# Kernel tuning notes

Measured on AMD Instinct MI355X. Metric: run time of the kernel, lower is better.

## Reference

```python
import jax, jax.numpy as jnp
import numpy as np

B, S, D = 2, 2048, 1024
H, HD = 16, 64          # num_heads, head_dim (D == H*HD)
FF = 4 * D
EPS = 1e-5

def _xavier(key, shape):
    fan_out, fan_in = shape
    lim = np.sqrt(6.0 / (fan_in + fan_out))
    return jax.random.uniform(key, shape, jnp.float32, -lim, lim)

def setup_inputs() -> dict:
    key = jax.random.key(0)
    ks = jax.random.split(key, 8)
    return {
        "x": jax.random.normal(ks[0], (B, S, D), jnp.float32),
        "g1": jnp.ones((D,), jnp.float32), "b1": jnp.zeros((D,), jnp.float32),
        "Wqkv": _xavier(ks[1], (3 * D, D)), "bqkv": jnp.zeros((3 * D,), jnp.float32),
        "Wo": _xavier(ks[2], (D, D)), "bo": jnp.zeros((D,), jnp.float32),
        "g2": jnp.ones((D,), jnp.float32), "b2": jnp.zeros((D,), jnp.float32),
        "W1": _xavier(ks[3], (FF, D)), "b1m": jnp.zeros((FF,), jnp.float32),
        "W2": _xavier(ks[4], (D, FF)), "b2m": jnp.zeros((D,), jnp.float32),
    }

def _ln(x, g, b):
    m = jnp.mean(x, axis=-1, keepdims=True)
    v = jnp.var(x, axis=-1, keepdims=True)
    return (x - m) * jax.lax.rsqrt(v + EPS) * g + b

def reference(x, g1, b1, Wqkv, bqkv, Wo, bo, g2, b2, W1, b1m, W2, b2m):
    # --- pre-norm attention ---
    h = _ln(x, g1, b1)
    qkv = h @ Wqkv.T + bqkv                                  # [B,S,3D]
    qkv = qkv.reshape(B, S, H, 3 * HD).transpose(0, 2, 1, 3)  # [B,H,S,3hd]
    q, k, v = jnp.split(qkv, 3, axis=-1)                      # each [B,H,S,hd]
    scores = jnp.einsum('bhqd,bhkd->bhqk', q, k) / np.sqrt(HD).astype(np.float32)
    att = jax.nn.softmax(scores, axis=-1)                     # [B,H,S,S]
    vals = jnp.einsum('bhqk,bhkd->bhqd', att, v)
    vals = vals.transpose(0, 2, 1, 3).reshape(B, S, D)
    x = x + (vals @ Wo.T + bo)
    # --- pre-norm MLP (dropouts inactive in eval) ---
    h = _ln(x, g2, b2)
    h = jax.nn.gelu(h @ W1.T + b1m, approximate=False)
    x = x + (h @ W2.T + b2m)
    return x
```

## Files before the change

kernel.cpp:

```cpp
#include <hip/hip_runtime.h>
#include <math.h>

#define BB 2
#define SS 2048
#define DD 1024
#define HH 16
#define FFDIM 4096
#define NROWS 4096

typedef short bf16x8 __attribute__((ext_vector_type(8)));
typedef float f32x4 __attribute__((ext_vector_type(4)));

__device__ __forceinline__ unsigned short f2bf(float f) {
    unsigned u = __float_as_uint(f);
    u += 0x7fffu + ((u >> 16) & 1u);
    return (unsigned short)(u >> 16);
}

typedef __attribute__((address_space(1))) void gvoid;
typedef __attribute__((address_space(3))) void lvoid;
__device__ __forceinline__ void glds16(const void* g, void* l) {
    __builtin_amdgcn_global_load_lds((gvoid*)g, (lvoid*)l, 16, 0, 0);
}

__device__ __forceinline__ int vkey(int kloc) {
    return (kloc & ~31) + ((kloc & 12) << 1) + ((kloc & 16) >> 2);
}

__global__ __launch_bounds__(256) void ln_kernel(const float* __restrict__ x,
                                                 const float* __restrict__ g,
                                                 const float* __restrict__ b,
                                                 unsigned short* __restrict__ out) {
    int row = blockIdx.x;
    const float* xr = x + (size_t)row * DD;
    unsigned short* orow = out + (size_t)row * DD;
    int t = threadIdx.x;
    float4 v = ((const float4*)xr)[t];
    float s  = v.x + v.y + v.z + v.w;
    float s2 = v.x*v.x + v.y*v.y + v.z*v.z + v.w*v.w;
    #pragma unroll
    for (int off = 32; off > 0; off >>= 1) {
        s  += __shfl_down(s,  off);
        s2 += __shfl_down(s2, off);
    }
    __shared__ float red1[4], red2[4];
    int wid = t >> 6, lane = t & 63;
    if (lane == 0) { red1[wid] = s; red2[wid] = s2; }
    __syncthreads();
    if (t == 0) {
        float a = 0.f, a2 = 0.f;
        #pragma unroll
        for (int i = 0; i < 4; ++i) { a += red1[i]; a2 += red2[i]; }
        red1[0] = a; red2[0] = a2;
    }
    __syncthreads();
    float mean = red1[0] * (1.0f / DD);
    float var  = red2[0] * (1.0f / DD) - mean * mean;
    float rs = rsqrtf(var + 1e-5f);
    float4 gv = ((const float4*)g)[t];
    float4 bv = ((const float4*)b)[t];
    ushort4 o;
    o.x = f2bf((v.x - mean) * rs * gv.x + bv.x);
    o.y = f2bf((v.y - mean) * rs * gv.y + bv.y);
    o.z = f2bf((v.z - mean) * rs * gv.z + bv.z);
    o.w = f2bf((v.w - mean) * rs * gv.w + bv.w);
    ((ushort4*)orow)[t] = o;
}

__global__ __launch_bounds__(256) void cast4(const float* __restrict__ a, unsigned short* __restrict__ oa,
                                             const float* __restrict__ b, unsigned short* __restrict__ ob,
                                             const float* __restrict__ c, unsigned short* __restrict__ oc,
                                             const float* __restrict__ d, unsigned short* __restrict__ od) {
    int i = blockIdx.x * 256 + threadIdx.x;
    const float* src; unsigned short* dst; int off;
    if (i < 786432)       { src = a; dst = oa; off = i; }
    else if (i < 1048576) { src = b; dst = ob; off = i - 786432; }
    else if (i < 2097152) { src = c; dst = oc; off = i - 1048576; }
    else                  { src = d; dst = od; off = i - 2097152; }
    float4 v = ((const float4*)src)[off];
    ushort4 o;
    o.x = f2bf(v.x); o.y = f2bf(v.y); o.z = f2bf(v.z); o.w = f2bf(v.w);
    ((ushort4*)dst)[off] = o;
}

template<int ACT, int RES, int OUTBF, int TN, int VT, int CS>
__global__ __launch_bounds__(256, 3) void gemm_nt_mfma(
    const unsigned short* __restrict__ A,
    const unsigned short* __restrict__ W,
    const float* __restrict__ bias,
    const float* __restrict__ res,
    void* __restrict__ Cout,
    unsigned short* __restrict__ Vtg,
    int M, int N, int K)
{
    constexpr int MI = (TN == 128) ? 4 : 2;
    constexpr int WR = TN / 4;
    __shared__ unsigned short SMEM[128 * 64 + TN * 64];
    unsigned short* As = SMEM;
    unsigned short* Ws = SMEM + 128 * 64;
    int tid = threadIdx.x;
    int lane = tid & 63;
    int w = tid >> 6;
    int rowbase = (TN == 128) ? ((w >> 1) * 64) : (w * 32);
    int colbase = (TN == 128) ? ((w & 1) * 64) : 0;
    int bm = blockIdx.y * 128, bn = blockIdx.x * TN;
    int col16 = lane & 15, quad = lane >> 4;

    f32x4 acc[MI][4] = {};

    int lrow = lane >> 3;
    int sw = (lane & 7) ^ lrow;
    const unsigned short* Ag = A + (size_t)(bm + w * 32 + lrow) * K + sw * 8;
    const unsigned short* Wg = W + (size_t)(bn + w * WR + lrow) * K + sw * 8;

    for (int k0 = 0; k0 < K; k0 += 64) {
        if (k0) __syncthreads();
        #pragma unroll
        for (int it = 0; it < 4; ++it)
            glds16(Ag + (size_t)(8 * it) * K + k0, &As[(w * 32 + 8 * it) * 64]);
        #pragma unroll
        for (int it = 0; it < WR / 8; ++it)
            glds16(Wg + (size_t)(8 * it) * K + k0, &Ws[(w * WR + 8 * it) * 64]);
        __syncthreads();
        #pragma unroll
        for (int c = 0; c < 2; ++c) {
            bf16x8 af[MI], bfr[4];
            #pragma unroll
            for (int i = 0; i < MI; ++i) {
                int m = rowbase + i * 16 + col16;
                af[i] = *(const bf16x8*)&As[m * 64 + (((c * 4 + quad) ^ (m & 7)) * 8)];
            }
            #pragma unroll
            for (int j = 0; j < 4; ++j) {
                int n = colbase + j * 16 + col16;
                bfr[j] = *(const bf16x8*)&Ws[n * 64 + (((c * 4 + quad) ^ (n & 7)) * 8)];
            }
            #pragma unroll
            for (int i = 0; i < MI; ++i)
                #pragma unroll
                for (int j = 0; j < 4; ++j)
                    acc[i][j] = __builtin_amdgcn_mfma_f32_16x16x32_bf16(af[i], bfr[j], acc[i][j], 0, 0, 0);
        }
    }

    if constexpr (CS) {
        __syncthreads();
        #pragma unroll
        for (int i = 0; i < MI; ++i) {
            #pragma unroll
            for (int j = 0; j < 4; ++j) {
                int nl = colbase + j * 16 + col16;
                float bv = bias[bn + nl];
                int c = nl >> 4;
                #pragma unroll
                for (int r = 0; r < 4; ++r) {
                    int ml = rowbase + i * 16 + quad * 4 + r;
                    float v = acc[i][j][r] + bv;
                    if (ACT) {
                        float z = v * (1.595769122f + 0.071354816f * v * v);
                        float e = __builtin_amdgcn_exp2f(-z * 1.442695041f);
                        v = v * __builtin_amdgcn_rcpf(1.0f + e);
                    }
                    SMEM[ml * 128 + ((c ^ ((ml >> 2) & 7)) << 4) + (nl & 15)] = f2bf(v);
                }
            }
        }
        __syncthreads();
        #pragma unroll
        for (int p = 0; p < 8; ++p) {
            int cid = tid + p * 256;
            int row = cid >> 4, cc = cid & 15;
            int cs2 = cc >> 1;
            bf16x8 vv = *(bf16x8*)&SMEM[row * 128 + ((cs2 ^ ((row >> 2) & 7)) << 4) + (cc & 1) * 8];
            *(bf16x8*)&((unsigned short*)Cout)[(size_t)(bm + row) * N + bn + cc * 8] = vv;
        }
        return;
    }

    bool wave_v = VT && ((((bn + colbase) >> 6) % 3) == 2);
    if constexpr (VT) __syncthreads();

    #pragma unroll
    for (int i = 0; i < MI; ++i) {
        #pragma unroll
        for (int j = 0; j < 4; ++j) {
            int nn = bn + colbase + j * 16 + col16;
            float bv = bias[nn];
            float vv[4];
            #pragma unroll
            for (int r = 0; r < 4; ++r) {
                float v = acc[i][j][r] + bv;
                if (ACT) {
                    float z = v * (1.595769122f + 0.071354816f * v * v);
                    float e = __builtin_amdgcn_exp2f(-z * 1.442695041f);
                    v = v * __builtin_amdgcn_rcpf(1.0f + e);
                }
                vv[r] = v;
            }
            int mm0 = bm + rowbase + i * 16 + quad * 4;
            if (VT && wave_v) {
                int d = j * 16 + col16;
                int kloc = rowbase + i * 16 + quad * 4;
                int vl = vkey(kloc);
                int ch = vl >> 3;
                ushort4 pk;
                pk.x = f2bf(vv[0]); pk.y = f2bf(vv[1]);
                pk.z = f2bf(vv[2]); pk.w = f2bf(vv[3]);
                *(ushort4*)&SMEM[d * 128 + ((ch ^ (d & 7)) << 3) + (vl & 7)] = pk;
            } else {
                #pragma unroll
                for (int r = 0; r < 4; ++r) {
                    int mm = mm0 + r;
                    float v = vv[r];
                    if (RES) v += res[(size_t)mm * N + nn];
                    if (OUTBF) ((unsigned short*)Cout)[(size_t)mm * N + nn] = f2bf(v);
                    else       ((float*)Cout)[(size_t)mm * N + nn] = v;
                }
            }
        }
    }

    if constexpr (VT) {
        __syncthreads();
        bool g0v = ((bn >> 6) % 3) == 2;
        bool g1v = (((bn + 64) >> 6) % 3) == 2;
        if (g0v || g1v) {
            int vcb = g0v ? 0 : 64;
            int hh = (bn + vcb) / 192;
            int bb = bm >> 11, sr = bm & 2047;
            #pragma unroll
            for (int p = 0; p < 4; ++p) {
                int cid = tid + p * 256;
                int d = cid >> 4, ch = cid & 15;
                bf16x8 vv2 = *(bf16x8*)&SMEM[d * 128 + ((ch ^ (d & 7)) << 3)];
                *(bf16x8*)&Vtg[((size_t)((bb * HH + hh) * 64 + d)) * (size_t)SS + sr + ch * 8] = vv2;
            }
        }
    }
}

__global__ __launch_bounds__(256, 4) void attn_mfma(
    const unsigned short* __restrict__ qkv,
    const unsigned short* __restrict__ Vtg,
    unsigned short* __restrict__ outb)
{
    __shared__ unsigned short Ks[128 * 64];
    __shared__ unsigned short VtL[64 * 128];
    int tid = threadIdx.x;
    int lane = tid & 63;
    int wv = tid >> 6;
    int qt = blockIdx.x, h = blockIdx.y, b = blockIdx.z;
    int col16 = lane & 15, quad = lane >> 4;

    const unsigned short* qbase = qkv + (size_t)(b * SS) * 3072;
    const unsigned short* Kg = qbase + h * 192 + 64;
    const unsigned short* Vg = Vtg + ((size_t)(b * HH + h) * 64) * (size_t)SS;

    const float C = 0.18033688011112042f;
    int qrow = qt * 64 + wv * 16 + col16;
    bf16x8 qf[2];
    qf[0] = *(const bf16x8*)&qbase[(size_t)qrow * 3072 + h * 192 + quad * 8];
    qf[1] = *(const bf16x8*)&qbase[(size_t)qrow * 3072 + h * 192 + 32 + quad * 8];
    #pragma unroll
    for (int c = 0; c < 2; ++c)
        #pragma unroll
        for (int i = 0; i < 8; ++i) {
            float f = __uint_as_float(((unsigned)(unsigned short)qf[c][i]) << 16) * C;
            qf[c][i] = (short)f2bf(f);
        }

    f32x4 o[4] = {};
    float lsum = 0.f;

    for (int s0 = 0; s0 < SS; s0 += 128) {
        if (s0) __syncthreads();
        #pragma unroll
        for (int p = 0; p < 4; ++p) {
            int ci = (p * 4 + wv) * 64 + lane;
            int k = ci >> 3, sk = ci & 7, qk = sk ^ (k & 7);
            glds16(Kg + (size_t)(s0 + k) * 3072 + qk * 8, &Ks[ci * 8]);
            int dv = ci >> 4, sv = ci & 15, qv = sv ^ (dv & 7);
            glds16(Vg + (size_t)dv * SS + s0 + qv * 8, &VtL[ci * 8]);
        }
        __syncthreads();

        f32x4 st[8];
        #pragma unroll
        for (int t = 0; t < 8; ++t) {
            f32x4 z = {};
            st[t] = z;
            int key = t * 16 + col16;
            #pragma unroll
            for (int c = 0; c < 2; ++c) {
                bf16x8 kf = *(const bf16x8*)&Ks[key * 64 + (((c * 4 + quad) ^ (key & 7)) * 8)];
                st[t] = __builtin_amdgcn_mfma_f32_16x16x32_bf16(kf, qf[c], st[t], 0, 0, 0);
            }
        }

        unsigned lo[8], hi[8];
        float psum = 0.f;
        #pragma unroll
        for (int t = 0; t < 8; ++t) {
            float p0 = __builtin_amdgcn_exp2f(st[t][0]);
            float p1 = __builtin_amdgcn_exp2f(st[t][1]);
            float p2 = __builtin_amdgcn_exp2f(st[t][2]);
            float p3 = __builtin_amdgcn_exp2f(st[t][3]);
            psum += (p0 + p1) + (p2 + p3);
            lo[t] = __builtin_amdgcn_perm(__float_as_uint(p1), __float_as_uint(p0), 0x07060302u);
            hi[t] = __builtin_amdgcn_perm(__float_as_uint(p3), __float_as_uint(p2), 0x07060302u);
        }
        psum += __shfl_xor(psum, 16);
        psum += __shfl_xor(psum, 32);
        lsum += psum;

        #pragma unroll
        for (int kc = 0; kc < 4; ++kc) {
            uint4 pk;
            pk.x = lo[2 * kc]; pk.y = hi[2 * kc];
            pk.z = lo[2 * kc + 1]; pk.w = hi[2 * kc + 1];
            bf16x8 pf = *(bf16x8*)&pk;
            #pragma unroll
            for (int nt = 0; nt < 4; ++nt) {
                int d = nt * 16 + col16;
                bf16x8 vf = *(const bf16x8*)&VtL[d * 128 + (((kc * 4 + quad) ^ (d & 7)) * 8)];
                o[nt] = __builtin_amdgcn_mfma_f32_16x16x32_bf16(pf, vf, o[nt], 0, 0, 0);
            }
        }
    }

    float linv = __builtin_amdgcn_rcpf(lsum);
    float linv_r[4];
    #pragma unroll
    for (int r = 0; r < 4; ++r) linv_r[r] = __shfl(linv, quad * 4 + r);

    int orow0 = b * SS + qt * 64 + wv * 16;
    #pragma unroll
    for (int r = 0; r < 4; ++r) {
        int mm = orow0 + quad * 4 + r;
        #pragma unroll
        for (int nt = 0; nt < 4; ++nt)
            outb[(size_t)mm * DD + h * 64 + nt * 16 + col16] = f2bf(o[nt][r] * linv_r[r]);
    }
}

extern "C" void kernel_launch(void* const* d_in, const int* in_sizes, int n_in,
                              void* d_out, int out_size, void* d_ws, size_t ws_size,
                              hipStream_t stream) {
    const float* x    = (const float*)d_in[0];
    const float* g1   = (const float*)d_in[1];
    const float* b1   = (const float*)d_in[2];
    const float* Wqkv = (const float*)d_in[3];
    const float* bqkv = (const float*)d_in[4];
    const float* Wo   = (const float*)d_in[5];
    const float* bo   = (const float*)d_in[6];
    const float* g2   = (const float*)d_in[7];
    const float* b2   = (const float*)d_in[8];
    const float* W1   = (const float*)d_in[9];
    const float* b1m  = (const float*)d_in[10];
    const float* W2   = (const float*)d_in[11];
    const float* b2m  = (const float*)d_in[12];
    float* out = (float*)d_out;

    char* wsb = (char*)d_ws;
    unsigned short* Wq_b  = (unsigned short*)(wsb);
    unsigned short* Wo_b  = (unsigned short*)(wsb + 6291456);
    unsigned short* W1_b  = (unsigned short*)(wsb + 8388608);
    unsigned short* W2_b  = (unsigned short*)(wsb + 16777216);
    unsigned short* hb    = (unsigned short*)(wsb + 25165824);
    unsigned short* qkvb  = (unsigned short*)(wsb + 33554432);
    unsigned short* attnb = (unsigned short*)(wsb + 58720256);
    float*          x1    = (float*)(wsb + 67108864);
    unsigned short* ffb   = (unsigned short*)(wsb + 83886080);
    unsigned short* Vtg   = (unsigned short*)(wsb + 83886080);

    cast4<<<12288, 256, 0, stream>>>(Wqkv, Wq_b, Wo, Wo_b, W1, W1_b, W2, W2_b);

    ln_kernel<<<NROWS, 256, 0, stream>>>(x, g1, b1, hb);
    gemm_nt_mfma<0,0,1,128,1,0><<<dim3(24, 32), 256, 0, stream>>>(hb, Wq_b, bqkv, nullptr, qkvb,
                                                                  Vtg, NROWS, 3 * DD, DD);
    attn_mfma<<<dim3(SS / 64, HH, BB), 256, 0, stream>>>(qkvb, Vtg, attnb);
    gemm_nt_mfma<0,1,0,64,0,0><<<dim3(16, 32), 256, 0, stream>>>(attnb, Wo_b, bo, x, x1,
                                                                 nullptr, NROWS, DD, DD);
    ln_kernel<<<NROWS, 256, 0, stream>>>(x1, g2, b2, hb);
    gemm_nt_mfma<1,0,1,128,0,1><<<dim3(32, 32), 256, 0, stream>>>(hb, W1_b, b1m, nullptr, ffb,
                                                                  nullptr, NROWS, FFDIM, DD);
    gemm_nt_mfma<0,1,0,64,0,0><<<dim3(16, 32), 256, 0, stream>>>(ffb, W2_b, b2m, x1, out,
                                                                 nullptr, NROWS, DD, FFDIM);
}
```

Measured before the change: 330.7 us.

## Split-K the W2 GEMM with a reduction kernel and double query rows per attention block

The final FFN down-projection (K=4096) now runs as a 2-way split-K GEMM with 128-wide tiles. It writes two fp32 partial buffers, and a new reduce_add kernel sums them with the residual and bias. This is meant to raise parallelism and per-block reuse on the long-K GEMM, at the cost of extra fp32 partial traffic and one more launch. Separately, the attention kernel now processes 128 query rows per block (two 64-row groups), so each K/V tile loaded into LDS is reused twice. The grid is halved and the occupancy hint drops to 2 blocks per CU.

```diff
diff --git a/kernel.cpp b/kernel.cpp
--- a/kernel.cpp
+++ b/kernel.cpp
@@ -83,13 +83,32 @@
     ((ushort4*)dst)[off] = o;
 }
 
-template<int ACT, int RES, int OUTBF, int TN, int VT, int CS>
+__global__ __launch_bounds__(256) void reduce_add(const float* __restrict__ x1,
+                                                  const float* __restrict__ P0,
+                                                  const float* __restrict__ P1,
+                                                  const float* __restrict__ bias,
+                                                  float* __restrict__ out) {
+    int i = blockIdx.x * 256 + threadIdx.x;
+    float4 a = ((const float4*)x1)[i];
+    float4 p = ((const float4*)P0)[i];
+    float4 q = ((const float4*)P1)[i];
+    float4 bv = ((const float4*)bias)[i & 255];
+    float4 o;
+    o.x = a.x + p.x + q.x + bv.x;
+    o.y = a.y + p.y + q.y + bv.y;
+    o.z = a.z + p.z + q.z + bv.z;
+    o.w = a.w + p.w + q.w + bv.w;
+    ((float4*)out)[i] = o;
+}
+
+template<int ACT, int RES, int OUTBF, int TN, int VT, int CS, int SPLITK>
 __global__ __launch_bounds__(256, 3) void gemm_nt_mfma(
     const unsigned short* __restrict__ A,
     const unsigned short* __restrict__ W,
     const float* __restrict__ bias,
     const float* __restrict__ res,
     void* __restrict__ Cout,
+    void* __restrict__ Cout2,
     unsigned short* __restrict__ Vtg,
     int M, int N, int K)
 {
@@ -106,6 +125,9 @@
     int bm = blockIdx.y * 128, bn = blockIdx.x * TN;
     int col16 = lane & 15, quad = lane >> 4;
 
+    int klen = SPLITK ? (K >> 1) : K;
+    int kbase = SPLITK ? ((int)blockIdx.z * klen) : 0;
+
     f32x4 acc[MI][4] = {};
 
     int lrow = lane >> 3;
@@ -113,8 +135,8 @@
     const unsigned short* Ag = A + (size_t)(bm + w * 32 + lrow) * K + sw * 8;
     const unsigned short* Wg = W + (size_t)(bn + w * WR + lrow) * K + sw * 8;
 
-    for (int k0 = 0; k0 < K; k0 += 64) {
-        if (k0) __syncthreads();
+    for (int k0 = kbase; k0 < kbase + klen; k0 += 64) {
+        if (k0 != kbase) __syncthreads();
         #pragma unroll
         for (int it = 0; it < 4; ++it)
             glds16(Ag + (size_t)(8 * it) * K + k0, &As[(w * 32 + 8 * it) * 64]);
@@ -141,6 +163,23 @@
                 for (int j = 0; j < 4; ++j)
                     acc[i][j] = __builtin_amdgcn_mfma_f32_16x16x32_bf16(af[i], bfr[j], acc[i][j], 0, 0, 0);
         }
+    }
+
+    if constexpr (SPLITK) {
+        float* P = (float*)(blockIdx.z ? Cout2 : Cout);
+        #pragma unroll
+        for (int i = 0; i < MI; ++i) {
+            #pragma unroll
+            for (int j = 0; j < 4; ++j) {
+                int nn = bn + colbase + j * 16 + col16;
+                #pragma unroll
+                for (int r = 0; r < 4; ++r) {
+                    int mm = bm + rowbase + i * 16 + quad * 4 + r;
+                    P[(size_t)mm * N + nn] = acc[i][j][r];
+                }
+            }
+        }
+        return;
     }
 
     if constexpr (CS) {
@@ -239,7 +278,7 @@
     }
 }
 
-__global__ __launch_bounds__(256, 4) void attn_mfma(
+__global__ __launch_bounds__(256, 2) void attn_mfma(
     const unsigned short* __restrict__ qkv,
     const unsigned short* __restrict__ Vtg,
     unsigned short* __restrict__ outb)
@@ -257,20 +296,23 @@
     const unsigned short* Vg = Vtg + ((size_t)(b * HH + h) * 64) * (size_t)SS;
 
     const float C = 0.18033688011112042f;
-    int qrow = qt * 64 + wv * 16 + col16;
-    bf16x8 qf[2];
-    qf[0] = *(const bf16x8*)&qbase[(size_t)qrow * 3072 + h * 192 + quad * 8];
-    qf[1] = *(const bf16x8*)&qbase[(size_t)qrow * 3072 + h * 192 + 32 + quad * 8];
+    bf16x8 qf[2][2];
     #pragma unroll
-    for (int c = 0; c < 2; ++c)
-        #pragma unroll
-        for (int i = 0; i < 8; ++i) {
-            float f = __uint_as_float(((unsigned)(unsigned short)qf[c][i]) << 16) * C;
-            qf[c][i] = (short)f2bf(f);
-        }
-
-    f32x4 o[4] = {};
-    float lsum = 0.f;
+    for (int qq = 0; qq < 2; ++qq) {
+        int qrow = qt * 128 + qq * 64 + wv * 16 + col16;
+        qf[qq][0] = *(const bf16x8*)&qbase[(size_t)qrow * 3072 + h * 192 + quad * 8];
+        qf[qq][1] = *(const bf16x8*)&qbase[(size_t)qrow * 3072 + h * 192 + 32 + quad * 8];
+        #pragma unroll
+        for (int c = 0; c < 2; ++c)
+            #pragma unroll
+            for (int i = 0; i < 8; ++i) {
+                float f = __uint_as_float(((unsigned)(unsigned short)qf[qq][c][i]) << 16) * C;
+                qf[qq][c][i] = (short)f2bf(f);
+            }
+    }
+
+    f32x4 o[2][4] = {};
+    float lsum[2] = {0.f, 0.f};
 
     for (int s0 = 0; s0 < SS; s0 += 128) {
         if (s0) __syncthreads();
@@ -284,62 +326,67 @@
         }
         __syncthreads();
 
-        f32x4 st[8];
-        #pragma unroll
-        for (int t = 0; t < 8; ++t) {
-            f32x4 z = {};
-            st[t] = z;
-            int key = t * 16 + col16;
-            #pragma unroll
-            for (int c = 0; c < 2; ++c) {
-                bf16x8 kf = *(const bf16x8*)&Ks[key * 64 + (((c * 4 + quad) ^ (key & 7)) * 8)];
-                st[t] = __builtin_amdgcn_mfma_f32_16x16x32_bf16(kf, qf[c], st[t], 0, 0, 0);
-            }
-        }
-
-        unsigned lo[8], hi[8];
-        float psum = 0.f;
-        #pragma unroll
-        for (int t = 0; t < 8; ++t) {
-            float p0 = __builtin_amdgcn_exp2f(st[t][0]);
-            float p1 = __builtin_amdgcn_exp2f(st[t][1]);
-            float p2 = __builtin_amdgcn_exp2f(st[t][2]);
-            float p3 = __builtin_amdgcn_exp2f(st[t][3]);
-            psum += (p0 + p1) + (p2 + p3);
-            lo[t] = __builtin_amdgcn_perm(__float_as_uint(p1), __float_as_uint(p0), 0x07060302u);
-            hi[t] = __builtin_amdgcn_perm(__float_as_uint(p3), __float_as_uint(p2), 0x07060302u);
-        }
-        psum += __shfl_xor(psum, 16);
-        psum += __shfl_xor(psum, 32);
-        lsum += psum;
-
-        #pragma unroll
-        for (int kc = 0; kc < 4; ++kc) {
-            uint4 pk;
-            pk.x = lo[2 * kc]; pk.y = hi[2 * kc];
-            pk.z = lo[2 * kc + 1]; pk.w = hi[2 * kc + 1];
-            bf16x8 pf = *(bf16x8*)&pk;
-            #pragma unroll
-            for (int nt = 0; nt < 4; ++nt) {
-                int d = nt * 16 + col16;
-                bf16x8 vf = *(const bf16x8*)&VtL[d * 128 + (((kc * 4 + quad) ^ (d & 7)) * 8)];
-                o[nt] = __builtin_amdgcn_mfma_f32_16x16x32_bf16(pf, vf, o[nt], 0, 0, 0);
-            }
-        }
-    }
-
-    float linv = __builtin_amdgcn_rcpf(lsum);
-    float linv_r[4];
+        #pragma unroll
+        for (int qq = 0; qq < 2; ++qq) {
+            f32x4 st[8];
+            #pragma unroll
+            for (int t = 0; t < 8; ++t) {
+                f32x4 z = {};
+                st[t] = z;
+                int key = t * 16 + col16;
+                #pragma unroll
+                for (int c = 0; c < 2; ++c) {
+                    bf16x8 kf = *(const bf16x8*)&Ks[key * 64 + (((c * 4 + quad) ^ (key & 7)) * 8)];
+                    st[t] = __builtin_amdgcn_mfma_f32_16x16x32_bf16(kf, qf[qq][c], st[t], 0, 0, 0);
+                }
+            }
+
+            unsigned lo[8], hi[8];
+            float psum = 0.f;
+            #pragma unroll
+            for (int t = 0; t < 8; ++t) {
+                float p0 = __builtin_amdgcn_exp2f(st[t][0]);
+                float p1 = __builtin_amdgcn_exp2f(st[t][1]);
+                float p2 = __builtin_amdgcn_exp2f(st[t][2]);
+                float p3 = __builtin_amdgcn_exp2f(st[t][3]);
+                psum += (p0 + p1) + (p2 + p3);
+                lo[t] = __builtin_amdgcn_perm(__float_as_uint(p1), __float_as_uint(p0), 0x07060302u);
+                hi[t] = __builtin_amdgcn_perm(__float_as_uint(p3), __float_as_uint(p2), 0x07060302u);
+            }
+            psum += __shfl_xor(psum, 16);
+            psum += __shfl_xor(psum, 32);
+            lsum[qq] += psum;
+
+            #pragma unroll
+            for (int kc = 0; kc < 4; ++kc) {
+                uint4 pk;
+                pk.x = lo[2 * kc]; pk.y = hi[2 * kc];
+                pk.z = lo[2 * kc + 1]; pk.w = hi[2 * kc + 1];
+                bf16x8 pf = *(bf16x8*)&pk;
+                #pragma unroll
+                for (int nt = 0; nt < 4; ++nt) {
+                    int d = nt * 16 + col16;
+                    bf16x8 vf = *(const bf16x8*)&VtL[d * 128 + (((kc * 4 + quad) ^ (d & 7)) * 8)];
+                    o[qq][nt] = __builtin_amdgcn_mfma_f32_16x16x32_bf16(pf, vf, o[qq][nt], 0, 0, 0);
+                }
+            }
+        }
+    }
+
     #pragma unroll
-    for (int r = 0; r < 4; ++r) linv_r[r] = __shfl(linv, quad * 4 + r);
-
-    int orow0 = b * SS + qt * 64 + wv * 16;
-    #pragma unroll
-    for (int r = 0; r < 4; ++r) {
-        int mm = orow0 + quad * 4 + r;
-        #pragma unroll
-        for (int nt = 0; nt < 4; ++nt)
-            outb[(size_t)mm * DD + h * 64 + nt * 16 + col16] = f2bf(o[nt][r] * linv_r[r]);
+    for (int qq = 0; qq < 2; ++qq) {
+        float linv = __builtin_amdgcn_rcpf(lsum[qq]);
+        float linv_r[4];
+        #pragma unroll
+        for (int r = 0; r < 4; ++r) linv_r[r] = __shfl(linv, quad * 4 + r);
+        int orow0 = b * SS + qt * 128 + qq * 64 + wv * 16;
+        #pragma unroll
+        for (int r = 0; r < 4; ++r) {
+            int mm = orow0 + quad * 4 + r;
+            #pragma unroll
+            for (int nt = 0; nt < 4; ++nt)
+                outb[(size_t)mm * DD + h * 64 + nt * 16 + col16] = f2bf(o[qq][nt][r] * linv_r[r]);
+        }
     }
 }
 
@@ -372,18 +419,21 @@
     float*          x1    = (float*)(wsb + 67108864);
     unsigned short* ffb   = (unsigned short*)(wsb + 83886080);
     unsigned short* Vtg   = (unsigned short*)(wsb + 83886080);
+    float*          P0    = (float*)(wsb + 33554432);
+    float*          P1    = (float*)(wsb + 50331648);
 
     cast4<<<12288, 256, 0, stream>>>(Wqkv, Wq_b, Wo, Wo_b, W1, W1_b, W2, W2_b);
 
     ln_kernel<<<NROWS, 256, 0, stream>>>(x, g1, b1, hb);
-    gemm_nt_mfma<0,0,1,128,1,0><<<dim3(24, 32), 256, 0, stream>>>(hb, Wq_b, bqkv, nullptr, qkvb,
-                                                                  Vtg, NROWS, 3 * DD, DD);
-    attn_mfma<<<dim3(SS / 64, HH, BB), 256, 0, stream>>>(qkvb, Vtg, attnb);
-    gemm_nt_mfma<0,1,0,64,0,0><<<dim3(16, 32), 256, 0, stream>>>(attnb, Wo_b, bo, x, x1,
-                                                                 nullptr, NROWS, DD, DD);
+    gemm_nt_mfma<0,0,1,128,1,0,0><<<dim3(24, 32), 256, 0, stream>>>(hb, Wq_b, bqkv, nullptr, qkvb,
+                                                                    nullptr, Vtg, NROWS, 3 * DD, DD);
+    attn_mfma<<<dim3(SS / 128, HH, BB), 256, 0, stream>>>(qkvb, Vtg, attnb);
+    gemm_nt_mfma<0,1,0,64,0,0,0><<<dim3(16, 32), 256, 0, stream>>>(attnb, Wo_b, bo, x, x1,
+                                                                   nullptr, nullptr, NROWS, DD, DD);
     ln_kernel<<<NROWS, 256, 0, stream>>>(x1, g2, b2, hb);
-    gemm_nt_mfma<1,0,1,128,0,1><<<dim3(32, 32), 256, 0, stream>>>(hb, W1_b, b1m, nullptr, ffb,
-                                                                  nullptr, NROWS, FFDIM, DD);
-    gemm_nt_mfma<0,1,0,64,0,0><<<dim3(16, 32), 256, 0, stream>>>(ffb, W2_b, b2m, x1, out,
-                                                                 nullptr, NROWS, DD, FFDIM);
-}
+    gemm_nt_mfma<1,0,1,128,0,1,0><<<dim3(32, 32), 256, 0, stream>>>(hb, W1_b, b1m, nullptr, ffb,
+                                                                    nullptr, nullptr, NROWS, FFDIM, DD);
+    gemm_nt_mfma<0,0,0,128,0,0,1><<<dim3(8, 32, 2), 256, 0, stream>>>(ffb, W2_b, nullptr, nullptr, P0,
+                                                                      P1, nullptr, NROWS, DD, FFDIM);
+    reduce_add<<<4096, 256, 0, stream>>>(x1, P0, P1, b2m, out);
+}
```

Result: no change. 327.5 us (-1.0%).
